# Performance work log

Hardware: AMD Instinct MI355X
Metric: run time of the kernel (lower is better)

## Reference

```python
import jax, jax.numpy as jnp
import numpy as np

NUM_KERNELS = 64
KERNEL_DIM = 16

def setup_inputs() -> dict:
    key = jax.random.key(0)
    kx, kt = jax.random.split(key)
    B, F = 512, 1024
    x = jax.random.normal(kx, (B, F), dtype=jnp.float32)
    # xavier_uniform for T: limit = sqrt(6/(fan_in+fan_out))
    fan_in, fan_out = F, NUM_KERNELS * KERNEL_DIM
    limit = float(np.sqrt(6.0 / (fan_in + fan_out)))
    T = jax.random.uniform(kt, (F, fan_out), dtype=jnp.float32, minval=-limit, maxval=limit)
    return {"x": x, "T": T}

def reference(x, T):
    B = x.shape[0]
    M = (x @ T).reshape(B, NUM_KERNELS, KERNEL_DIM)          # [B, K, D]
    # all-pairs L1 distance over D: [B, B, K]
    l1 = jnp.abs(M[None, :, :, :] - M[:, None, :, :]).sum(axis=3)
    Kmat = jnp.exp(-l1)                                        # [B, B, K]
    return Kmat.sum(axis=1) - 1.0                              # [B, K]
```

## Files before the change

### kernel.cpp

```cpp
#include <hip/hip_runtime.h>
#include <hip/hip_fp16.h>

#define BB 512
#define FF 1024
#define NK 64
#define KD 16

typedef __attribute__((ext_vector_type(4))) float f32x4;
typedef __attribute__((ext_vector_type(8))) _Float16 half8;
typedef __attribute__((ext_vector_type(8))) unsigned short ushort8;

__device__ __forceinline__ unsigned short f16_bits(float f) {
    __half h = __float2half(f);
    return *reinterpret_cast<unsigned short*>(&h);
}

__global__ __launch_bounds__(256) void md_mfma_fused_kernel(
    const float* __restrict__ x, const float* __restrict__ T,
    float* __restrict__ M2, float* __restrict__ out) {
    __shared__ __align__(16) unsigned short lds[2][4096];

    const int t = threadIdx.x, w = t >> 6, l = t & 63;
    const int b = blockIdx.x, xc = b & 7, r = b >> 3;
    const int nt = xc * 4 + (r & 3);
    const int mt = r >> 2;

    if (b < 4) {
        const float4 z = make_float4(0.f, 0.f, 0.f, 0.f);
        #pragma unroll
        for (int q = 0; q < 8; ++q)
            *(float4*)&out[(size_t)(b * 2048 + q * 256 + t) * 4] = z;
    }

    const int rowA = t >> 3, k8 = t & 7;
    const float* gA = x + (size_t)(mt * 32 + rowA) * FF + k8 * 8;
    const int wA = rowA * 64 + ((k8 ^ (rowA & 7)) * 8);

    const int k2 = (t >> 3) * 2, nB = (t & 7) * 4;
    const float* gB = T + (size_t)k2 * FF + nt * 32 + nB;
    const int c16B = ((k2 >> 3) * 8) ;

    const int lrow = l & 15, lkg = l >> 4;
    const int ar = (w >> 1) * 16 + lrow;
    const int br = (w & 1) * 16 + lrow;
    const int swa = ar & 7, swb = br & 7;

    f32x4 acc = {};
    float4 a0[2], a1[2], b0[2], b1[2];

#define LOADT(s, it_) do {                                                  \
        a0[s] = *(const float4*)(gA + (it_) * 64);                          \
        a1[s] = *(const float4*)(gA + (it_) * 64 + 4);                      \
        b0[s] = *(const float4*)(gB + (size_t)(it_) * 64 * FF);             \
        b1[s] = *(const float4*)(gB + (size_t)(it_) * 64 * FF + FF);        \
    } while (0)

#define CVTW(s, bf) do {                                                    \
        ushort8 hv;                                                         \
        hv[0] = f16_bits(a0[s].x); hv[1] = f16_bits(a0[s].y);               \
        hv[2] = f16_bits(a0[s].z); hv[3] = f16_bits(a0[s].w);               \
        hv[4] = f16_bits(a1[s].x); hv[5] = f16_bits(a1[s].y);               \
        hv[6] = f16_bits(a1[s].z); hv[7] = f16_bits(a1[s].w);               \
        *(ushort8*)&lds[bf][wA] = hv;                                       \
        const float q0[4] = {b0[s].x, b0[s].y, b0[s].z, b0[s].w};           \
        const float q1[4] = {b1[s].x, b1[s].y, b1[s].z, b1[s].w};           \
        _Pragma("unroll")                                                   \
        for (int j = 0; j < 4; ++j) {                                       \
            const unsigned int pk = (unsigned int)f16_bits(q0[j]) |         \
                                    ((unsigned int)f16_bits(q1[j]) << 16);  \
            const int n = nB + j;                                           \
            *(unsigned int*)&lds[bf][2048 + n * 64 +                        \
                (c16B ^ ((n & 7) * 8)) + (k2 & 7)] = pk;                    \
        }                                                                   \
    } while (0)

    LOADT(0, 0);
    LOADT(1, 1);
    CVTW(0, 0);
    __syncthreads();

    #pragma unroll
    for (int it = 0; it < 16; ++it) {
        const int s = it & 1;
        if (it + 2 < 16) LOADT(s, it + 2);
        const unsigned short* L = lds[s];
        #pragma unroll
        for (int ks = 0; ks < 2; ++ks) {
            const int cb = ks * 4 + lkg;
            const half8 af = *(const half8*)&L[ar * 64 + ((cb ^ swa) * 8)];
            const half8 bf = *(const half8*)&L[2048 + br * 64 + ((cb ^ swb) * 8)];
            acc = __builtin_amdgcn_mfma_f32_16x16x32_f16(af, bf, acc, 0, 0, 0);
        }
        if (it + 1 < 16) {
            CVTW(s ^ 1, s ^ 1);
            __syncthreads();
        }
    }
#undef LOADT
#undef CVTW

    const int kblk = nt * 2 + (w & 1);
    const int rowb = mt * 32 + (w >> 1) * 16 + lkg * 4;
    #pragma unroll
    for (int rg = 0; rg < 4; ++rg)
        M2[((size_t)kblk * BB + rowb + rg) * KD + lrow] = acc[rg];
}

__global__ __launch_bounds__(256) void md_pairwise_sym_kernel(
    const float* __restrict__ M2, float* __restrict__ out) {
    __shared__ float Mj[64][16];
    __shared__ float et[64][65];
    __shared__ float part_row[4][64];
    __shared__ float part_col[4][64];

    const int bx = blockIdx.x;
    const int k = bx & 63;
    int p = bx >> 6;
    int it = 0;
    while (p >= 8 - it) { p -= 8 - it; ++it; }
    const int jt = it + p;
    const bool diag = (it == jt);
    const int t = threadIdx.x;

    const float* tileI = M2 + ((size_t)k * BB + it * 64) * KD;
    const float* tileJ = M2 + ((size_t)k * BB + jt * 64) * KD;

    {
        const int row = t >> 2, dg = (t & 3) * 4;
        *(float4*)&Mj[row][dg] = *(const float4*)&tileJ[t * 4];
    }

    const int i = t & 63;
    const int wv = t >> 6;

    float mi[16];
    #pragma unroll
    for (int dg = 0; dg < 4; ++dg) {
        const float4 v = *(const float4*)&tileI[i * KD + dg * 4];
        mi[dg * 4 + 0] = v.x; mi[dg * 4 + 1] = v.y;
        mi[dg * 4 + 2] = v.z; mi[dg * 4 + 3] = v.w;
    }
    __syncthreads();

    float row_acc = 0.0f;
    #pragma unroll 4
    for (int jj = 0; jj < 16; ++jj) {
        const int j = wv * 16 + jj;
        const float4* mj = (const float4*)&Mj[j][0];
        const float4 v0 = mj[0], v1 = mj[1], v2 = mj[2], v3 = mj[3];
        float p0 = (fabsf(mi[0] - v0.x) + fabsf(mi[1] - v0.y)) +
                   (fabsf(mi[2] - v0.z) + fabsf(mi[3] - v0.w));
        float p1 = (fabsf(mi[4] - v1.x) + fabsf(mi[5] - v1.y)) +
                   (fabsf(mi[6] - v1.z) + fabsf(mi[7] - v1.w));
        float p2 = (fabsf(mi[8] - v2.x) + fabsf(mi[9] - v2.y)) +
                   (fabsf(mi[10] - v2.z) + fabsf(mi[11] - v2.w));
        float p3 = (fabsf(mi[12] - v3.x) + fabsf(mi[13] - v3.y)) +
                   (fabsf(mi[14] - v3.z) + fabsf(mi[15] - v3.w));
        const float e = __expf(-((p0 + p1) + (p2 + p3)));
        row_acc += e;
        et[i][j] = e;
    }
    part_row[wv][i] = row_acc;
    __syncthreads();

    if (!diag) {
        const int j = t & 63;
        const int chunk = t >> 6;
        float col_acc = 0.0f;
        #pragma unroll
        for (int ii = 0; ii < 16; ++ii)
            col_acc += et[chunk * 16 + ii][j];
        part_col[chunk][j] = col_acc;
    }
    __syncthreads();

    if (t < 64) {
        float r = ((part_row[0][t] + part_row[1][t]) +
                   (part_row[2][t] + part_row[3][t])) - (diag ? 1.0f : 0.0f);
        atomicAdd(&out[(size_t)(it * 64 + t) * NK + k], r);
    } else if (t < 128 && !diag) {
        const int j = t - 64;
        float c = (part_col[0][j] + part_col[1][j]) +
                  (part_col[2][j] + part_col[3][j]);
        atomicAdd(&out[(size_t)(jt * 64 + j) * NK + k], c);
    }
}

extern "C" void kernel_launch(void* const* d_in, const int* in_sizes, int n_in,
                              void* d_out, int out_size, void* d_ws, size_t ws_size,
                              hipStream_t stream) {
    const float* x = (const float*)d_in[0];
    const float* T = (const float*)d_in[1];
    float* out = (float*)d_out;

    float* M2 = (float*)d_ws;

    md_mfma_fused_kernel<<<dim3(512), 256, 0, stream>>>(x, T, M2, out);
    md_pairwise_sym_kernel<<<dim3(36 * 64), 256, 0, stream>>>(M2, out);
}
```

Measured before the change: 30.96 us.

## Replace symmetric tile pairwise kernel with full-row kernel using scalar broadcast loads

Result: slower. 32.53 us (+5.0%).

```diff
diff --git a/kernel.cpp b/kernel.cpp
--- a/kernel.cpp
+++ b/kernel.cpp
@@ -17,7 +17,7 @@
 
 __global__ __launch_bounds__(256) void md_mfma_fused_kernel(
     const float* __restrict__ x, const float* __restrict__ T,
-    float* __restrict__ M2, float* __restrict__ out) {
+    float* __restrict__ M2) {
     __shared__ __align__(16) unsigned short lds[2][4096];
 
     const int t = threadIdx.x, w = t >> 6, l = t & 63;
@@ -25,20 +25,13 @@
     const int nt = xc * 4 + (r & 3);
     const int mt = r >> 2;
 
-    if (b < 4) {
-        const float4 z = make_float4(0.f, 0.f, 0.f, 0.f);
-        #pragma unroll
-        for (int q = 0; q < 8; ++q)
-            *(float4*)&out[(size_t)(b * 2048 + q * 256 + t) * 4] = z;
-    }
-
     const int rowA = t >> 3, k8 = t & 7;
     const float* gA = x + (size_t)(mt * 32 + rowA) * FF + k8 * 8;
     const int wA = rowA * 64 + ((k8 ^ (rowA & 7)) * 8);
 
     const int k2 = (t >> 3) * 2, nB = (t & 7) * 4;
     const float* gB = T + (size_t)k2 * FF + nt * 32 + nB;
-    const int c16B = ((k2 >> 3) * 8) ;
+    const int c16B = ((k2 >> 3) * 8);
 
     const int lrow = l & 15, lkg = l >> 4;
     const int ar = (w >> 1) * 16 + lrow;
@@ -106,48 +99,38 @@
         M2[((size_t)kblk * BB + rowb + rg) * KD + lrow] = acc[rg];
 }
 
-__global__ __launch_bounds__(256) void md_pairwise_sym_kernel(
+__global__ __launch_bounds__(512) void md_pairwise_kernel(
     const float* __restrict__ M2, float* __restrict__ out) {
-    __shared__ float Mj[64][16];
-    __shared__ float et[64][65];
-    __shared__ float part_row[4][64];
-    __shared__ float part_col[4][64];
+    __shared__ float part[8][64];
 
-    const int bx = blockIdx.x;
-    const int k = bx & 63;
-    int p = bx >> 6;
-    int it = 0;
-    while (p >= 8 - it) { p -= 8 - it; ++it; }
-    const int jt = it + p;
-    const bool diag = (it == jt);
-    const int t = threadIdx.x;
+    const int b = blockIdx.x;
+    const int xcd = b & 7, rest = b >> 3;
+    const int k = xcd * 8 + (rest & 7);
+    const int it = rest >> 3;
+    const int t = threadIdx.x, wv = t >> 6, i = t & 63;
 
-    const float* tileI = M2 + ((size_t)k * BB + it * 64) * KD;
-    const float* tileJ = M2 + ((size_t)k * BB + jt * 64) * KD;
+    const float* col = M2 + (size_t)k * (BB * KD);
 
+    float mi[16];
     {
-        const int row = t >> 2, dg = (t & 3) * 4;
-        *(float4*)&Mj[row][dg] = *(const float4*)&tileJ[t * 4];
+        const float* mip = col + (size_t)(it * 64 + i) * KD;
+        #pragma unroll
+        for (int dg = 0; dg < 4; ++dg) {
+            const float4 v = *(const float4*)(mip + dg * 4);
+            mi[dg * 4 + 0] = v.x; mi[dg * 4 + 1] = v.y;
+            mi[dg * 4 + 2] = v.z; mi[dg * 4 + 3] = v.w;
+        }
     }
 
-    const int i = t & 63;
-    const int wv = t >> 6;
-
-    float mi[16];
-    #pragma unroll
-    for (int dg = 0; dg < 4; ++dg) {
-        const float4 v = *(const float4*)&tileI[i * KD + dg * 4];
-        mi[dg * 4 + 0] = v.x; mi[dg * 4 + 1] = v.y;
-        mi[dg * 4 + 2] = v.z; mi[dg * 4 + 3] = v.w;
-    }
-    __syncthreads();
-
-    float row_acc = 0.0f;
-    #pragma unroll 4
-    for (int jj = 0; jj < 16; ++jj) {
-        const int j = wv * 16 + jj;
-        const float4* mj = (const float4*)&Mj[j][0];
-        const float4 v0 = mj[0], v1 = mj[1], v2 = mj[2], v3 = mj[3];
+    float acc = 0.0f;
+    const int j0 = wv * 64;
+    #pragma unroll 2
+    for (int jj = 0; jj < 64; ++jj) {
+        const int off = __builtin_amdgcn_readfirstlane((j0 + jj) * KD);
+        const float4 v0 = *(const float4*)(col + off);
+        const float4 v1 = *(const float4*)(col + off + 4);
+        const float4 v2 = *(const float4*)(col + off + 8);
+        const float4 v3 = *(const float4*)(col + off + 12);
         float p0 = (fabsf(mi[0] - v0.x) + fabsf(mi[1] - v0.y)) +
                    (fabsf(mi[2] - v0.z) + fabsf(mi[3] - v0.w));
         float p1 = (fabsf(mi[4] - v1.x) + fabsf(mi[5] - v1.y)) +
@@ -156,33 +139,15 @@
                    (fabsf(mi[10] - v2.z) + fabsf(mi[11] - v2.w));
         float p3 = (fabsf(mi[12] - v3.x) + fabsf(mi[13] - v3.y)) +
                    (fabsf(mi[14] - v3.z) + fabsf(mi[15] - v3.w));
-        const float e = __expf(-((p0 + p1) + (p2 + p3)));
-        row_acc += e;
-        et[i][j] = e;
+        acc += __expf(-((p0 + p1) + (p2 + p3)));
     }
-    part_row[wv][i] = row_acc;
+
+    part[wv][i] = acc;
     __syncthreads();
-
-    if (!diag) {
-        const int j = t & 63;
-        const int chunk = t >> 6;
-        float col_acc = 0.0f;
-        #pragma unroll
-        for (int ii = 0; ii < 16; ++ii)
-            col_acc += et[chunk * 16 + ii][j];
-        part_col[chunk][j] = col_acc;
-    }
-    __syncthreads();
-
     if (t < 64) {
-        float r = ((part_row[0][t] + part_row[1][t]) +
-                   (part_row[2][t] + part_row[3][t])) - (diag ? 1.0f : 0.0f);
-        atomicAdd(&out[(size_t)(it * 64 + t) * NK + k], r);
-    } else if (t < 128 && !diag) {
-        const int j = t - 64;
-        float c = (part_col[0][j] + part_col[1][j]) +
-                  (part_col[2][j] + part_col[3][j]);
-        atomicAdd(&out[(size_t)(jt * 64 + j) * NK + k], c);
+        const float s = ((part[0][t] + part[1][t]) + (part[2][t] + part[3][t])) +
+                        ((part[4][t] + part[5][t]) + (part[6][t] + part[7][t])) - 1.0f;
+        out[(size_t)(it * 64 + t) * NK + k] = s;
     }
 }
 
@@ -195,6 +160,6 @@
 
     float* M2 = (float*)d_ws;
 
-    md_mfma_fused_kernel<<<dim3(512), 256, 0, stream>>>(x, T, M2, out);
-    md_pairwise_sym_kernel<<<dim3(36 * 64), 256, 0, stream>>>(M2, out);
+    md_mfma_fused_kernel<<<dim3(512), 256, 0, stream>>>(x, T, M2);
+    md_pairwise_kernel<<<dim3(512), 512, 0, stream>>>(M2, out);
 }
```
